# Kernel optimization log

Hardware: AMD Instinct MI355X
Metric: run time of the kernel (lower is better)

The kernel has to match this reference:

```python
import jax, jax.numpy as jnp
import numpy as np

EPS_S = 1e-06
EPS_SUM = 1e-08
EPS_LOG = 1e-08


def gram_eigh_svd(h_flat):
    """h_flat: (B, N, k) float32 -> (S: (B,k) desc, Vh: (B,k,k)).
    SVD of h_flat via eigendecomposition of the k x k gram matrix."""
    G = jnp.einsum('bnk,bnm->bkm', h_flat, h_flat)  # (B, k, k)
    evals, evecs = jnp.linalg.eigh(G)               # ascending eigenvalues
    S = jnp.sqrt(jnp.clip(evals, 0.0, None))[:, ::-1]          # descending
    Vh = jnp.swapaxes(evecs[:, :, ::-1], -2, -1)                # rows = right singular vectors
    return S, Vh


def extract_features(S, Vh):
    """(B,k), (B,k,k) -> (B, 2k+2)."""
    S_safe = jnp.clip(S, EPS_S, None)
    s_norm = S_safe / (jnp.sum(S_safe, axis=-1, keepdims=True) + EPS_SUM)
    vh_diag = jnp.diagonal(Vh, axis1=-2, axis2=-1)                       # (B, k)
    vh_offdiag = jnp.clip(
        jnp.sum(Vh * Vh, axis=(-2, -1)) - jnp.sum(vh_diag * vh_diag, axis=-1),
        0.0, None)[:, None]                                              # (B, 1)
    s_ent = -jnp.sum(s_norm * jnp.log(jnp.clip(s_norm, EPS_LOG, None)),
                     axis=-1, keepdims=True)                             # (B, 1)
    out = jnp.concatenate([s_norm, vh_diag, vh_offdiag, s_ent], axis=-1)
    return jnp.where(jnp.isfinite(out), out, jnp.zeros_like(out))


def setup_inputs() -> dict:
    key = jax.random.key(0)
    k1, k2 = jax.random.split(key)
    B, C, H, W = 64, 512, 64, 64
    k = 24
    x = jax.random.normal(k1, (B, C, H, W), dtype=jnp.float32)
    w_proj = jax.random.normal(k2, (k, C), dtype=jnp.float32) * (1.0 / np.sqrt(C))
    ema_s = jnp.ones((k,), dtype=jnp.float32)
    return {"x": x, "w_proj": w_proj, "ema_s": ema_s}


def reference(x, w_proj, ema_s):
    B, C, H, W = x.shape
    k = w_proj.shape[0]
    # 1x1 conv == per-pixel matmul; go straight to (B, H*W, k)
    h_flat = jnp.einsum('bchw,kc->bhwk', x, w_proj).reshape(B, H * W, k)
    # torch path runs eigh under no_grad / fp32
    S, Vh = gram_eigh_svd(jax.lax.stop_gradient(h_flat.astype(jnp.float32)))
    S = jnp.clip(S, EPS_S, None)
    S = jnp.where(jnp.isfinite(S), S, jnp.ones_like(S))
    Vh = jnp.where(jnp.isfinite(Vh), Vh, jnp.zeros_like(Vh))
    features = extract_features(S, Vh)
    novelty = S - ema_s[None, :]
    return (S, Vh, features, novelty)
```

## Files before the change

kernel.cpp:

```cpp
#include <hip/hip_runtime.h>
#include <math.h>


#define N24 24
#define ZST 65
#define HS 25

__global__ __launch_bounds__(256, 1) void proj_gram_kernel(
    const float* __restrict__ x, const float* __restrict__ w,
    double* __restrict__ partial)
{
    const int b    = blockIdx.x >> 2;
    const int q    = blockIdx.x & 3;
    const int tid  = threadIdx.x;
    const int wv   = tid >> 6;
    const int lane = tid & 63;
    const int n0   = (q << 10) | (tid << 2);
    __shared__ __align__(16) float wl[24 * 512];
    __shared__ float hl[4][256 * HS];
    for (int i2 = tid; i2 < 24 * 512; i2 += 256) wl[i2] = w[i2];
    __syncthreads();

    const float* xb = x + ((size_t)b << 21) + n0;
    float h[4][24];
#pragma unroll
    for (int j = 0; j < 4; ++j)
#pragma unroll
        for (int k = 0; k < 24; ++k) h[j][k] = 0.f;

    float4 cA[16];
#pragma unroll
    for (int t = 0; t < 16; ++t)
        cA[t] = *reinterpret_cast<const float4*>(xb + ((size_t)t << 12));

    for (int c = 0; c < 512; c += 16) {
        float4 cB[16];
        if (c + 16 < 512) {
#pragma unroll
            for (int t = 0; t < 16; ++t)
                cB[t] = *reinterpret_cast<const float4*>(xb + ((size_t)(c + 16 + t) << 12));
        }
#pragma unroll
        for (int sub = 0; sub < 4; ++sub) {
            const float4 a0 = cA[sub * 4 + 0];
            const float4 a1 = cA[sub * 4 + 1];
            const float4 a2 = cA[sub * 4 + 2];
            const float4 a3 = cA[sub * 4 + 3];
            const int cc = c + sub * 4;
#pragma unroll
            for (int k = 0; k < 24; ++k) {
                const float4 wv4 = *reinterpret_cast<const float4*>(&wl[k * 512 + cc]);
                h[0][k] += wv4.x * a0.x + wv4.y * a1.x + wv4.z * a2.x + wv4.w * a3.x;
                h[1][k] += wv4.x * a0.y + wv4.y * a1.y + wv4.z * a2.y + wv4.w * a3.y;
                h[2][k] += wv4.x * a0.z + wv4.y * a1.z + wv4.z * a2.z + wv4.w * a3.z;
                h[3][k] += wv4.x * a0.w + wv4.y * a1.w + wv4.z * a2.w + wv4.w * a3.w;
            }
        }
#pragma unroll
        for (int t = 0; t < 16; ++t) cA[t] = cB[t];
    }

    float* hq = hl[wv];
#pragma unroll
    for (int j = 0; j < 4; ++j)
#pragma unroll
        for (int k = 0; k < 24; ++k)
            hq[((lane << 2) + j) * HS + k] = h[j][k];

    for (int p = lane; p < 300; p += 64) {
        int k = 0, pp = p;
        while (pp >= 24 - k) { pp -= 24 - k; ++k; }
        int m = k + pp;
        double acc = 0.0;
        for (int i2 = 0; i2 < 256; ++i2)
            acc += (double)hq[i2 * HS + k] * (double)hq[i2 * HS + m];
        partial[((size_t)(b * 16 + (q << 2) + wv)) * 300 + p] = acc;
    }
}

__global__ __launch_bounds__(320) void gram_reduce_kernel(
    const double* __restrict__ partial, float* __restrict__ G)
{
    const int b = blockIdx.x;
    const int p = threadIdx.x;
    if (p >= 300) return;
    int k = 0, pp = p;
    while (pp >= 24 - k) { pp -= 24 - k; ++k; }
    int m = k + pp;
    double acc = 0.0;
    for (int t = 0; t < 16; ++t)
        acc += partial[((size_t)(b * 16 + t)) * 300 + p];
    float v = (float)acc;
    G[b * 576 + k * 24 + m] = v;
    G[b * 576 + m * 24 + k] = v;
}

__device__ __forceinline__ float rlf(float v, int l) {
    return __int_as_float(__builtin_amdgcn_readlane(__float_as_int(v), l));
}

__device__ __forceinline__ float lapy2f(float xx, float yy) {
#pragma clang fp contract(off)
    float xa = fabsf(xx), ya = fabsf(yy);
    float w = fmaxf(xa, ya), z = fminf(xa, ya);
    float q = z / w;
    float res = w * sqrtf(1.f + q * q);
    return (z == 0.f) ? w : res;
}

__device__ __forceinline__ void slartg_(float f, float g, float& c, float& s, float& r) {
#pragma clang fp contract(off)
    float f1 = fabsf(f), g1 = fabsf(g);
    const float rtmin_ = 0x1p-63f;
    const float rtmax_ = 1.8446743e+19f;
    bool inr = (f1 > rtmin_) && (f1 < rtmax_) && (g1 > rtmin_) && (g1 < rtmax_);
    if (__builtin_expect(!inr && f != 0.f && g != 0.f, 0)) {
        float u = fminf(3.4028235e+38f, fmaxf(0x1p-126f, fmaxf(f1, g1)));
        float fs = f / u, gs = g / u;
        float d = sqrtf(fs * fs + gs * gs);
        float p = 1.f / d;
        c = fabsf(fs) * p;
        s = gs * copysignf(p, f);
        r = copysignf(d, f) * u;
    } else {
        float d = sqrtf(f * f + g * g);
        float p = 1.f / d;
        float cN = f1 * p;
        float sN = g * copysignf(p, f);
        float rN = copysignf(d, f);
        bool gz = (g == 0.f), fz = (f == 0.f);
        c = gz ? 1.f : (fz ? 0.f : cN);
        s = gz ? 0.f : (fz ? copysignf(1.f, g) : sN);
        r = gz ? f   : (fz ? g1 : rN);
    }
}

__device__ __forceinline__ void slaev2_(float a, float b, float cc,
                                        float& rt1, float& rt2, float& cs1, float& sn1) {
#pragma clang fp contract(off)
    float sm = a + cc, df = a - cc, adf = fabsf(df);
    float tb = b + b, ab = fabsf(tb);
    float acmx, acmn;
    if (fabsf(a) > fabsf(cc)) { acmx = a; acmn = cc; } else { acmx = cc; acmn = a; }
    float rt;
    if (adf > ab)      { float q = ab / adf; rt = adf * sqrtf(1.f + q * q); }
    else if (adf < ab) { float q = adf / ab; rt = ab * sqrtf(1.f + q * q); }
    else               rt = ab * sqrtf(2.f);
    int sgn1;
    if (sm < 0.f)      { rt1 = 0.5f * (sm - rt); sgn1 = -1; rt2 = (acmx / rt1) * acmn - (b / rt1) * b; }
    else if (sm > 0.f) { rt1 = 0.5f * (sm + rt); sgn1 =  1; rt2 = (acmx / rt1) * acmn - (b / rt1) * b; }
    else               { rt1 = 0.5f * rt; rt2 = -0.5f * rt; sgn1 = 1; }
    float cs; int sgn2;
    if (df >= 0.f) { cs = df + rt; sgn2 = 1; } else { cs = df - rt; sgn2 = -1; }
    float acs = fabsf(cs);
    if (acs > ab) { float ct = -tb / cs; sn1 = 1.f / sqrtf(1.f + ct * ct); cs1 = ct * sn1; }
    else {
        if (ab == 0.f) { cs1 = 1.f; sn1 = 0.f; }
        else { float tn = -cs / tb; cs1 = 1.f / sqrtf(1.f + tn * tn); sn1 = tn * cs1; }
    }
    if (sgn1 == sgn2) { float tn = cs1; cs1 = -sn1; sn1 = tn; }
}

#define RD(j)   rlf(dr, (j) - 1)
#define RE(j)   rlf(er, (j) - 1)
#define WD(j,v) { float _v = (v); int _j = (j) - 1; dr = (lane == _j) ? _v : dr; }
#define WE(j,v) { float _v = (v); int _j = (j) - 1; er = (lane == _j) ? _v : er; }

__global__ __launch_bounds__(64) void eigh_feat_kernel(
    const float* __restrict__ G, const float* __restrict__ ema,
    float* __restrict__ out)
{
#pragma clang fp contract(off)
    const int b = blockIdx.x;
    const int lane = threadIdx.x;
    const int n = N24;

    __shared__ float A[N24 * N24];
    __shared__ float Zl[ZST * N24];
    __shared__ float dl[N24 + 1], el[N24 + 1], tau[N24 + 1];
    __shared__ float hv[N24], hw[N24];
    __shared__ float Sarr[N24], snorm[N24];

    for (int idx = lane; idx < n * n; idx += 64) A[idx] = G[(size_t)b * n * n + idx];
    __syncthreads();

    for (int i = 0; i < n - 1; ++i) {
        const int mlen = n - 1 - i;
        float alpha = A[(i + 1) + N24 * i];
        float ss = 0.f;
        for (int r = i + 2; r < n; ++r) { float t = A[r + N24 * i]; ss += t * t; }
        float xnorm = sqrtf(ss);
        if (xnorm == 0.f) {
            if (lane == 0) { tau[i + 1] = 0.f; el[i + 1] = alpha; dl[i + 1] = A[i + N24 * i]; }
            __syncthreads();
            continue;
        }
        float beta = -copysignf(lapy2f(alpha, xnorm), alpha);
        float taui = (beta - alpha) / beta;
        float scal = 1.f / (alpha - beta);
        if (lane == 0) { tau[i + 1] = taui; el[i + 1] = beta; }
        __syncthreads();
        if (lane >= i + 2 && lane < n) A[lane + N24 * i] *= scal;
        __syncthreads();
        if (lane < mlen) hv[lane] = (lane == 0) ? 1.f : A[(i + 1 + lane) + N24 * i];
        __syncthreads();
        if (lane < mlen) {
            float acc = 0.f;
            int gr = i + 1 + lane;
            for (int c2 = 0; c2 < mlen; ++c2) {
                int gc = i + 1 + c2;
                float av = (gr >= gc) ? A[gr + N24 * gc] : A[gc + N24 * gr];
                acc += av * hv[c2];
            }
            hw[lane] = taui * acc;
        }
        __syncthreads();
        float dot = 0.f;
        for (int r2 = 0; r2 < mlen; ++r2) dot += hw[r2] * hv[r2];
        float alpha2 = -0.5f * taui * dot;
        __syncthreads();
        if (lane < mlen) hw[lane] += alpha2 * hv[lane];
        __syncthreads();
        if (lane < mlen) {
            for (int c2 = 0; c2 <= lane; ++c2)
                A[(i + 1 + lane) + N24 * (i + 1 + c2)] -= hv[lane] * hw[c2] + hw[lane] * hv[c2];
        }
        __syncthreads();
        if (lane == 0) dl[i + 1] = A[i + N24 * i];
        __syncthreads();
    }
    if (lane == 0) dl[n] = A[(n - 1) + N24 * (n - 1)];
    __syncthreads();

#pragma unroll
    for (int j = 0; j < N24; ++j) Zl[lane + ZST * j] = (lane == j) ? 1.f : 0.f;

    float dr = (lane < 24) ? dl[lane + 1] : 0.f;
    float er = (lane < 23) ? el[lane + 1] : 0.f;

    {
        const float eps_    = 0x1p-24f;
        const float eps2_   = 0x1p-48f;
        const float safmin_ = 0x1p-126f;
        const float ssfmax_ = 3.0744573e+18f;
        const float ssfmin_ = 0x1p-15f;
        const int nmaxit = n * 30;
        int jtot = 0, l1 = 1;
        int l = 0, lsv = 0, lend = 0, lendsv = 0, mb = 0, iscale = 0;
        float anorm = 0.f, p = 0.f, g = 0.f, r_ = 0.f, c_ = 0.f, s_ = 0.f, f_ = 0.f, b_ = 0.f;
        float rt1 = 0.f, rt2 = 0.f, cc = 0.f, sn = 0.f;
        int m_ = 0, i_ = 0;

L10:
        if (l1 > n) goto L160;
        if (l1 > 1) WE(l1 - 1, 0.f);
        {
            float dnx = __shfl_down(dr, 1, 64);
            float ae = fabsf(er);
            bool inr = (lane >= l1 - 1) && (lane <= n - 2);
            bool t0 = inr && (ae == 0.f);
            bool t1 = inr && (ae <= (sqrtf(fabsf(dr)) * sqrtf(fabsf(dnx))) * eps_);
            unsigned long long msk0 = __ballot(t0);
            unsigned long long mskc = msk0 | __ballot(t1);
            if (mskc) {
                int bit = __builtin_ctzll(mskc);
                m_ = bit + 1;
                bool wasz = (msk0 >> bit) & 1ull;
                if (!wasz) WE(m_, 0.f);
            } else m_ = n;
        }
        l = l1; lsv = l; lend = m_; lendsv = lend; l1 = m_ + 1;
        if (lend == l) goto L10;

        {
            bool ind = (lane >= l - 1) && (lane <= lend - 1);
            bool ine = (lane >= l - 1) && (lane <= lend - 2);
            float v = fmaxf(ind ? fabsf(dr) : 0.f, ine ? fabsf(er) : 0.f);
            for (int off = 32; off; off >>= 1) v = fmaxf(v, __shfl_xor(v, off, 64));
            anorm = v;
        }
        iscale = 0;
        if (anorm == 0.f) goto L10;
        if (anorm > ssfmax_) {
            iscale = 1;
            float mul = ssfmax_ / anorm;
            if (lane + 1 >= l && lane + 1 <= lend) dr *= mul;
            if (lane + 1 >= l && lane + 1 <= lend - 1) er *= mul;
        } else if (anorm < ssfmin_) {
            iscale = 2;
            float mul = ssfmin_ / anorm;
            if (lane + 1 >= l && lane + 1 <= lend) dr *= mul;
            if (lane + 1 >= l && lane + 1 <= lend - 1) er *= mul;
        }
        if (fabsf(RD(lend)) < fabsf(RD(l))) { lend = lsv; l = lendsv; }

        if (lend > l) {
L40:
            if (l != lend) {
                float dnx = __shfl_down(dr, 1, 64);
                bool inr = (lane >= l - 1) && (lane <= lend - 2);
                bool t = inr && (er * er <= (eps2_ * fabsf(dr)) * fabsf(dnx) + safmin_);
                unsigned long long msk = __ballot(t);
                m_ = msk ? (__builtin_ctzll(msk) + 1) : lend;
            } else m_ = lend;
            if (m_ < lend) WE(m_, 0.f);
            mb = m_;
            p = RD(l);
            if (mb == l) goto L80;
            if (mb == l + 1) {
                slaev2_(RD(l), RE(l), RD(l + 1), rt1, rt2, cc, sn);
                {
                    float z1 = Zl[lane + ZST * l];
                    float z0 = Zl[lane + ZST * (l - 1)];
                    Zl[lane + ZST * l]       = cc * z1 - sn * z0;
                    Zl[lane + ZST * (l - 1)] = sn * z1 + cc * z0;
                }
                WD(l, rt1); WD(l + 1, rt2); WE(l, 0.f);
                l = l + 2;
                if (l <= lend) goto L40;
                goto L140;
            }
            if (jtot == nmaxit) goto L140;
            jtot = jtot + 1;
            {
                float dmb = RD(mb);
                g = (RD(l + 1) - p) / (2.f * RE(l));
                r_ = lapy2f(g, 1.f);
                g = dmb - p + (RE(l) / (g + copysignf(r_, g)));
                s_ = 1.f; c_ = 1.f; p = 0.f;
                float dcar = dmb;
                float carry = Zl[lane + ZST * (mb - 1)];
                for (i_ = mb - 1; i_ >= l; --i_) {
                    float prev = Zl[lane + ZST * (i_ - 1)];
                    float ei = RE(i_);
                    float di = RD(i_);
                    f_ = s_ * ei;
                    b_ = c_ * ei;
                    slartg_(g, f_, c_, s_, r_);
                    er = ((i_ != mb - 1) && (lane == i_)) ? r_ : er;
                    g = dcar - p;
                    r_ = (di - g) * s_ + 2.f * c_ * b_;
                    p = s_ * r_;
                    dr = (lane == i_) ? (g + p) : dr;
                    g = c_ * r_ - b_;
                    dcar = di;
                    float sj = -s_;
                    Zl[lane + ZST * i_] = c_ * carry - sj * prev;
                    carry = sj * carry + c_ * prev;
                }
                Zl[lane + ZST * (l - 1)] = carry;
                WD(l, dcar - p);
                WE(l, g);
            }
            goto L40;
L80:
            WD(l, p);
            l = l + 1;
            if (l <= lend) goto L40;
            goto L140;
        } else {
L90:
            if (l != lend) {
                float epu = __shfl_up(er, 1, 64);
                float dup = __shfl_up(dr, 1, 64);
                bool inr = (lane >= lend) && (lane <= l - 1);
                bool t = inr && (epu * epu <= (eps2_ * fabsf(dr)) * fabsf(dup) + safmin_);
                unsigned long long msk = __ballot(t);
                if (msk) {
                    m_ = 63 - __builtin_clzll(msk) + 1;
                } else m_ = lend;
            } else m_ = lend;
            if (m_ > lend) WE(m_ - 1, 0.f);
            mb = m_;
            p = RD(l);
            if (mb == l) goto L130;
            if (mb == l - 1) {
                slaev2_(RD(l - 1), RE(l - 1), RD(l), rt1, rt2, cc, sn);
                {
                    float z1 = Zl[lane + ZST * (l - 1)];
                    float z0 = Zl[lane + ZST * (l - 2)];
                    Zl[lane + ZST * (l - 1)] = cc * z1 - sn * z0;
                    Zl[lane + ZST * (l - 2)] = sn * z1 + cc * z0;
                }
                WD(l - 1, rt1); WD(l, rt2); WE(l - 1, 0.f);
                l = l - 2;
                if (l >= lend) goto L90;
                goto L140;
            }
            if (jtot == nmaxit) goto L140;
            jtot = jtot + 1;
            {
                float dmb = RD(mb);
                g = (RD(l - 1) - p) / (2.f * RE(l - 1));
                r_ = lapy2f(g, 1.f);
                g = dmb - p + (RE(l - 1) / (g + copysignf(r_, g)));
                s_ = 1.f; c_ = 1.f; p = 0.f;
                float dcar = dmb;
                float carryPrev = Zl[lane + ZST * (mb - 1)];
                for (i_ = mb; i_ <= l - 1; ++i_) {
                    float t = Zl[lane + ZST * i_];
                    float ei = RE(i_);
                    float dnx = RD(i_ + 1);
                    f_ = s_ * ei;
                    b_ = c_ * ei;
                    slartg_(g, f_, c_, s_, r_);
                    er = ((i_ != mb) && (lane == i_ - 2)) ? r_ : er;
                    g = dcar - p;
                    r_ = (dnx - g) * s_ + 2.f * c_ * b_;
                    p = s_ * r_;
                    dr = (lane == i_ - 1) ? (g + p) : dr;
                    g = c_ * r_ - b_;
                    dcar = dnx;
                    Zl[lane + ZST * (i_ - 1)] = s_ * t + c_ * carryPrev;
                    carryPrev = c_ * t - s_ * carryPrev;
                }
                Zl[lane + ZST * (l - 1)] = carryPrev;
                WD(l, dcar - p);
                WE(l - 1, g);
            }
            goto L90;
L130:
            WD(l, p);
            l = l - 1;
            if (l >= lend) goto L90;
            goto L140;
        }
L140:
        if (iscale == 1) {
            float mul = anorm / ssfmax_;
            if (lane + 1 >= lsv && lane + 1 <= lendsv) dr *= mul;
            if (lane + 1 >= lsv && lane + 1 <= lendsv - 1) er *= mul;
        } else if (iscale == 2) {
            float mul = anorm / ssfmin_;
            if (lane + 1 >= lsv && lane + 1 <= lendsv) dr *= mul;
            if (lane + 1 >= lsv && lane + 1 <= lendsv - 1) er *= mul;
        }
        if (jtot < nmaxit) goto L10;
        goto L160;

L160:
        for (int ii = 2; ii <= n; ++ii) {
            int ia = ii - 1;
            float val = (lane >= ii - 2 && lane <= n - 1) ? dr : __builtin_inff();
            int idx = lane + 1;
            for (int off = 32; off; off >>= 1) {
                float v2 = __shfl_xor(val, off, 64);
                int   i2 = __shfl_xor(idx, off, 64);
                bool take = (v2 < val) || ((v2 == val) && (i2 < idx));
                val = take ? v2 : val;
                idx = take ? i2 : idx;
            }
            int ka = idx;
            float pp = val;
            if (ka != ia) {
                float dia = RD(ia);
                WD(ka, dia);
                WD(ia, pp);
                {
                    float t = Zl[lane + ZST * (ia - 1)];
                    Zl[lane + ZST * (ia - 1)] = Zl[lane + ZST * (ka - 1)];
                    Zl[lane + ZST * (ka - 1)] = t;
                }
            }
        }
    }

    if (lane < 24) dl[lane + 1] = dr;
    __syncthreads();

    for (int i = n - 2; i >= 0; --i) {
        float taui = tau[i + 1];
        if (taui != 0.f && lane < n) {
            int j = lane;
            float w_ = Zl[(i + 1) + ZST * j];
            for (int r = i + 2; r < n; ++r) w_ += A[r + N24 * i] * Zl[r + ZST * j];
            Zl[(i + 1) + ZST * j] -= taui * w_;
            for (int r = i + 2; r < n; ++r) Zl[r + ZST * j] -= taui * (A[r + N24 * i] * w_);
        }
        __syncthreads();
    }

    const int S_OFF = 0, VH_OFF = 1536, F_OFF = 38400, NOV_OFF = 41600;
    if (lane < n) {
        float ev = dl[n - lane];
        float s0 = sqrtf(fmaxf(ev, 0.f));
        s0 = fmaxf(s0, 1e-6f);
        if (!isfinite(s0)) s0 = 1.f;
        Sarr[lane] = s0;
    }
    __syncthreads();
    if (lane < n) {
        out[S_OFF + b * 24 + lane] = Sarr[lane];
        out[NOV_OFF + b * 24 + lane] = Sarr[lane] - ema[lane];
    }
    for (int idx = lane; idx < 576; idx += 64) {
        int j = idx / 24, i2 = idx % 24;
        float vv = Zl[i2 + ZST * (23 - j)];
        if (!isfinite(vv)) vv = 0.f;
        out[VH_OFF + b * 576 + idx] = vv;
    }
    float sum_ = 0.f;
    for (int j2 = 0; j2 < n; ++j2) sum_ += Sarr[j2];
    float denom = sum_ + 1e-8f;
    if (lane < n) snorm[lane] = Sarr[lane] / denom;
    __syncthreads();
    float ent = 0.f;
    for (int j2 = 0; j2 < n; ++j2) {
        float sn2 = snorm[j2];
        ent -= sn2 * logf(fmaxf(sn2, 1e-8f));
    }
    float sumsq = 0.f, diagsq = 0.f;
    for (int j2 = 0; j2 < n; ++j2)
        for (int i2 = 0; i2 < n; ++i2) { float z = Zl[i2 + ZST * j2]; sumsq += z * z; }
    for (int j2 = 0; j2 < n; ++j2) { float dv = Zl[j2 + ZST * (23 - j2)]; diagsq += dv * dv; }
    float offd = fmaxf(sumsq - diagsq, 0.f);
    if (lane < n) {
        float v0 = snorm[lane]; if (!isfinite(v0)) v0 = 0.f;
        out[F_OFF + b * 50 + lane] = v0;
        float dv = Zl[lane + ZST * (23 - lane)]; if (!isfinite(dv)) dv = 0.f;
        out[F_OFF + b * 50 + 24 + lane] = dv;
    }
    if (lane == 0) {
        if (!isfinite(offd)) offd = 0.f;
        if (!isfinite(ent)) ent = 0.f;
        out[F_OFF + b * 50 + 48] = offd;
        out[F_OFF + b * 50 + 49] = ent;
    }
}

extern "C" void kernel_launch(void* const* d_in, const int* in_sizes, int n_in,
                              void* d_out, int out_size, void* d_ws, size_t ws_size,
                              hipStream_t stream)
{
    const float* x   = (const float*)d_in[0];
    const float* w   = (const float*)d_in[1];
    const float* ema = (const float*)d_in[2];
    float* out = (float*)d_out;

    char* wsb = (char*)d_ws;
    double* partial = (double*)(wsb + 0);
    float*  G       = (float*)(wsb + 2457600);

    hipLaunchKernelGGL(proj_gram_kernel, dim3(256), dim3(256), 0, stream, x, w, partial);
    hipLaunchKernelGGL(gram_reduce_kernel, dim3(64), dim3(320), 0, stream, partial, G);
    hipLaunchKernelGGL(eigh_feat_kernel, dim3(64), dim3(64), 0, stream, G, ema, out);
}
```

Baseline: 475.7 us.

## Double projection grid, halve per-thread pixels, fold gram reduce into eigh kernel

The projection-gram kernel now runs 512 blocks, with each thread handling 2 pixels instead of 4 and loading float2 instead of float4. This cuts registers and allows 2 blocks per CU, so more of the GPU's CUs are busy. Each wave builds its partial gram in two 32-lane halves through a smaller shared buffer and accumulates 5 pairs per lane in registers. The separate reduce kernel is removed; the eigh kernel now sums 32 double partials per batch and fills the symmetric matrix itself. This saves one launch, but the reduction work moves into a 64-block, single-wave kernel.

```diff
diff --git a/kernel.cpp b/kernel.cpp
--- a/kernel.cpp
+++ b/kernel.cpp
@@ -6,93 +6,100 @@
 #define ZST 65
 #define HS 25
 
-__global__ __launch_bounds__(256, 1) void proj_gram_kernel(
+__global__ __launch_bounds__(256, 2) void proj_gram_kernel(
     const float* __restrict__ x, const float* __restrict__ w,
     double* __restrict__ partial)
 {
-    const int b    = blockIdx.x >> 2;
-    const int q    = blockIdx.x & 3;
+    const int b    = blockIdx.x >> 3;
+    const int q    = blockIdx.x & 7;
     const int tid  = threadIdx.x;
     const int wv   = tid >> 6;
     const int lane = tid & 63;
-    const int n0   = (q << 10) | (tid << 2);
+    const int n0   = (q << 9) | (tid << 1);
     __shared__ __align__(16) float wl[24 * 512];
-    __shared__ float hl[4][256 * HS];
+    __shared__ float hq[4][64 * HS];
     for (int i2 = tid; i2 < 24 * 512; i2 += 256) wl[i2] = w[i2];
     __syncthreads();
 
     const float* xb = x + ((size_t)b << 21) + n0;
-    float h[4][24];
-#pragma unroll
-    for (int j = 0; j < 4; ++j)
+    float h[2][24];
+#pragma unroll
+    for (int j = 0; j < 2; ++j)
 #pragma unroll
         for (int k = 0; k < 24; ++k) h[j][k] = 0.f;
 
-    float4 cA[16];
-#pragma unroll
-    for (int t = 0; t < 16; ++t)
-        cA[t] = *reinterpret_cast<const float4*>(xb + ((size_t)t << 12));
-
-    for (int c = 0; c < 512; c += 16) {
-        float4 cB[16];
-        if (c + 16 < 512) {
-#pragma unroll
-            for (int t = 0; t < 16; ++t)
-                cB[t] = *reinterpret_cast<const float4*>(xb + ((size_t)(c + 16 + t) << 12));
-        }
-#pragma unroll
-        for (int sub = 0; sub < 4; ++sub) {
-            const float4 a0 = cA[sub * 4 + 0];
-            const float4 a1 = cA[sub * 4 + 1];
-            const float4 a2 = cA[sub * 4 + 2];
-            const float4 a3 = cA[sub * 4 + 3];
+    float2 cA[8];
+#pragma unroll
+    for (int t = 0; t < 8; ++t)
+        cA[t] = *reinterpret_cast<const float2*>(xb + ((size_t)t << 12));
+
+    for (int c = 0; c < 512; c += 8) {
+        float2 cB[8];
+        if (c + 8 < 512) {
+#pragma unroll
+            for (int t = 0; t < 8; ++t)
+                cB[t] = *reinterpret_cast<const float2*>(xb + ((size_t)(c + 8 + t) << 12));
+        }
+#pragma unroll
+        for (int sub = 0; sub < 2; ++sub) {
+            const float2 a0 = cA[sub * 4 + 0];
+            const float2 a1 = cA[sub * 4 + 1];
+            const float2 a2 = cA[sub * 4 + 2];
+            const float2 a3 = cA[sub * 4 + 3];
             const int cc = c + sub * 4;
 #pragma unroll
             for (int k = 0; k < 24; ++k) {
                 const float4 wv4 = *reinterpret_cast<const float4*>(&wl[k * 512 + cc]);
                 h[0][k] += wv4.x * a0.x + wv4.y * a1.x + wv4.z * a2.x + wv4.w * a3.x;
                 h[1][k] += wv4.x * a0.y + wv4.y * a1.y + wv4.z * a2.y + wv4.w * a3.y;
-                h[2][k] += wv4.x * a0.z + wv4.y * a1.z + wv4.z * a2.z + wv4.w * a3.z;
-                h[3][k] += wv4.x * a0.w + wv4.y * a1.w + wv4.z * a2.w + wv4.w * a3.w;
-            }
-        }
-#pragma unroll
-        for (int t = 0; t < 16; ++t) cA[t] = cB[t];
-    }
-
-    float* hq = hl[wv];
-#pragma unroll
-    for (int j = 0; j < 4; ++j)
-#pragma unroll
-        for (int k = 0; k < 24; ++k)
-            hq[((lane << 2) + j) * HS + k] = h[j][k];
-
-    for (int p = lane; p < 300; p += 64) {
+            }
+        }
+#pragma unroll
+        for (int t = 0; t < 8; ++t) cA[t] = cB[t];
+    }
+
+    float* hr = hq[wv];
+    int pk[5], pm[5];
+#pragma unroll
+    for (int u = 0; u < 5; ++u) {
+        int p = lane + u * 64;
         int k = 0, pp = p;
-        while (pp >= 24 - k) { pp -= 24 - k; ++k; }
-        int m = k + pp;
-        double acc = 0.0;
-        for (int i2 = 0; i2 < 256; ++i2)
-            acc += (double)hq[i2 * HS + k] * (double)hq[i2 * HS + m];
-        partial[((size_t)(b * 16 + (q << 2) + wv)) * 300 + p] = acc;
-    }
-}
-
-__global__ __launch_bounds__(320) void gram_reduce_kernel(
-    const double* __restrict__ partial, float* __restrict__ G)
-{
-    const int b = blockIdx.x;
-    const int p = threadIdx.x;
-    if (p >= 300) return;
-    int k = 0, pp = p;
-    while (pp >= 24 - k) { pp -= 24 - k; ++k; }
-    int m = k + pp;
-    double acc = 0.0;
-    for (int t = 0; t < 16; ++t)
-        acc += partial[((size_t)(b * 16 + t)) * 300 + p];
-    float v = (float)acc;
-    G[b * 576 + k * 24 + m] = v;
-    G[b * 576 + m * 24 + k] = v;
+        if (p < 300) {
+            while (pp >= 24 - k) { pp -= 24 - k; ++k; }
+        }
+        pk[u] = k; pm[u] = k + pp;
+    }
+    double acc[5];
+#pragma unroll
+    for (int u = 0; u < 5; ++u) acc[u] = 0.0;
+
+    for (int r = 0; r < 2; ++r) {
+        if ((lane >> 5) == r) {
+            int base = lane - (r << 5);
+#pragma unroll
+            for (int j = 0; j < 2; ++j)
+#pragma unroll
+                for (int k = 0; k < 24; ++k)
+                    hr[((base << 1) + j) * HS + k] = h[j][k];
+        }
+        __builtin_amdgcn_wave_barrier();
+#pragma unroll
+        for (int u = 0; u < 5; ++u) {
+            if (lane + u * 64 < 300) {
+                double a = acc[u];
+                for (int i2 = 0; i2 < 64; ++i2)
+                    a += (double)hr[i2 * HS + pk[u]] * (double)hr[i2 * HS + pm[u]];
+                acc[u] = a;
+            }
+        }
+        __builtin_amdgcn_wave_barrier();
+    }
+#pragma unroll
+    for (int u = 0; u < 5; ++u) {
+        int p = lane + u * 64;
+        if (p < 300)
+            partial[((size_t)(b * 32 + (q << 2) + wv)) * 300 + p] = acc[u];
+    }
 }
 
 __device__ __forceinline__ float rlf(float v, int l) {
@@ -167,7 +174,7 @@
 #define WE(j,v) { float _v = (v); int _j = (j) - 1; er = (lane == _j) ? _v : er; }
 
 __global__ __launch_bounds__(64) void eigh_feat_kernel(
-    const float* __restrict__ G, const float* __restrict__ ema,
+    const double* __restrict__ partial, const float* __restrict__ ema,
     float* __restrict__ out)
 {
 #pragma clang fp contract(off)
@@ -181,7 +188,17 @@
     __shared__ float hv[N24], hw[N24];
     __shared__ float Sarr[N24], snorm[N24];
 
-    for (int idx = lane; idx < n * n; idx += 64) A[idx] = G[(size_t)b * n * n + idx];
+    for (int p = lane; p < 300; p += 64) {
+        int k = 0, pp = p;
+        while (pp >= 24 - k) { pp -= 24 - k; ++k; }
+        int m = k + pp;
+        double acc = 0.0;
+        for (int t = 0; t < 32; ++t)
+            acc += partial[((size_t)(b * 32 + t)) * 300 + p];
+        float v = (float)acc;
+        A[k + N24 * m] = v;
+        A[m + N24 * k] = v;
+    }
     __syncthreads();
 
     for (int i = 0; i < n - 1; ++i) {
@@ -537,11 +554,8 @@
     const float* ema = (const float*)d_in[2];
     float* out = (float*)d_out;
 
-    char* wsb = (char*)d_ws;
-    double* partial = (double*)(wsb + 0);
-    float*  G       = (float*)(wsb + 2457600);
-
-    hipLaunchKernelGGL(proj_gram_kernel, dim3(256), dim3(256), 0, stream, x, w, partial);
-    hipLaunchKernelGGL(gram_reduce_kernel, dim3(64), dim3(320), 0, stream, partial, G);
-    hipLaunchKernelGGL(eigh_feat_kernel, dim3(64), dim3(64), 0, stream, G, ema, out);
-}
+    double* partial = (double*)d_ws;
+
+    hipLaunchKernelGGL(proj_gram_kernel, dim3(512), dim3(256), 0, stream, x, w, partial);
+    hipLaunchKernelGGL(eigh_feat_kernel, dim3(64), dim3(64), 0, stream, partial, ema, out);
+}
```

New measurement: 456.8 us. -4.0%, faster.
